# Performance work log

Hardware: AMD Instinct MI355X
Metric: run time of the kernel (lower is better)

Reference implementation:

```python
import jax, jax.numpy as jnp
import numpy as np

B, C, H, W = 2, 256, 48, 48
KD = 256          # key_dim
CLS = 20          # num_classes
NT = H * W        # patch tokens in query
N = CLS + NT      # key length (cls tokens + patches)
HDS = 8           # num_heads
HD = C // HDS     # head_dim
SCALE = HD ** -0.5
MR = 0.3          # mask_ratio
EPS = 1e-5


def setup_inputs() -> dict:
    key = jax.random.key(0)
    ks = jax.random.split(key, 10)
    s = 0.02
    return {
        "x_query": jax.random.normal(ks[0], (B, C, H, W), jnp.float32),
        "x_key": jax.random.normal(ks[1], (B, N, KD), jnp.float32),
        "mask_u": jax.random.uniform(ks[2], (B, HDS, N, N), jnp.float32),
        "g1": jnp.ones((C,), jnp.float32), "be1": jnp.zeros((C,), jnp.float32),
        "g2": jnp.ones((KD,), jnp.float32), "be2": jnp.zeros((KD,), jnp.float32),
        "g3": jnp.ones((C,), jnp.float32), "be3": jnp.zeros((C,), jnp.float32),
        "Wq": jax.random.normal(ks[3], (C, C), jnp.float32) * s,
        "Wkv": jax.random.normal(ks[4], (KD, 2 * C), jnp.float32) * s,
        "Wcls": jax.random.normal(ks[5], (KD, C), jnp.float32) * s,
        "Wp": jax.random.normal(ks[6], (C, C), jnp.float32) * s,
        "bp": jnp.zeros((C,), jnp.float32),
        "W1": jax.random.normal(ks[7], (C, 4 * C), jnp.float32) * s,
        "bf1": jnp.zeros((4 * C,), jnp.float32),
        "W2": jax.random.normal(ks[8], (4 * C, C), jnp.float32) * s,
        "bf2": jnp.zeros((C,), jnp.float32),
    }


def _ln(x, g, b):
    m = jnp.mean(x, -1, keepdims=True)
    v = jnp.mean((x - m) ** 2, -1, keepdims=True)
    return (x - m) * jax.lax.rsqrt(v + EPS) * g + b


def reference(x_query, x_key, mask_u, g1, be1, g2, be2, g3, be3,
              Wq, Wkv, Wcls, Wp, bp, W1, bf1, W2, bf2):
    Bb, Cc, Hh, Ww = x_query.shape
    xq = x_query.transpose(0, 2, 3, 1).reshape(Bb, -1, Cc)  # [B, Nt, C]
    q_in = _ln(xq, g1, be1)
    k_in = _ln(x_key, g2, be2)
    # cross attention with cls-token prepend
    cls_t = k_in[:, :CLS] @ Wcls                      # [B, Cls, C]
    qcat = jnp.concatenate([cls_t, q_in @ Wq], 1)     # [B, Cls+Nt, C]
    M = qcat.shape[1]
    Nk = x_key.shape[1]
    q = qcat.reshape(Bb, M, HDS, HD).transpose(0, 2, 1, 3)        # [B,h,M,d]
    kv = (k_in @ Wkv).reshape(Bb, Nk, 2, HDS, HD).transpose(2, 0, 3, 1, 4)
    k, v = kv[0], kv[1]                                           # [B,h,N,d]
    attn = jnp.einsum('bhmd,bhnd->bhmn', q, k) * SCALE            # [B,h,M,N]
    # split softmax: cls columns and patch columns normalized separately
    attn = jnp.concatenate([
        jax.nn.softmax(attn[..., :CLS], axis=-1),
        jax.nn.softmax(attn[..., CLS:], axis=-1),
    ], axis=-1)
    # stochastic bernoulli(mask_ratio) mask -> -1e12, then re-softmax
    bern = (mask_u < MR).astype(attn.dtype)
    attn = jax.nn.softmax(attn + bern * (-1e12), axis=-1)
    x = jnp.einsum('bhmn,bhnd->bhmd', attn, v)
    x = x.transpose(0, 2, 1, 3).reshape(Bb, M, Cc)
    x = x @ Wp + bp
    x = x[:, CLS:]                                    # drop cls rows
    xq = xq + x                                       # residual 1
    h = jax.nn.gelu(_ln(xq, g3, be3) @ W1 + bf1, approximate=False)
    xq = xq + (h @ W2 + bf2)                          # residual 2 (MLP)
    return xq.transpose(0, 2, 1).reshape(Bb, Cc, Hh, Ww)
```

## Files before the change

kernel.cpp:

```cpp
#include <hip/hip_runtime.h>
#include <hip/hip_bf16.h>
#include <cstddef>

#define B_ 2
#define C_ 256
#define HW_ 2304
#define CLS_ 20
#define N_ 2324
#define HDS_ 8
#define HD_ 32
#define SCALE_F 0.17677669529663687f
#define MR_ 0.3f
#define EPS_ 1e-5f
#define NT64 37
#define NPAD 2368

typedef __attribute__((ext_vector_type(8))) short short8;
typedef __attribute__((ext_vector_type(4))) float f32x4;
typedef unsigned long long u64;

__device__ __forceinline__ short f2bf(float x) {
    union { __hip_bfloat16 b; short s; } u;
    u.b = __float2bfloat16(x);
    return u.s;
}
__device__ __forceinline__ u64 shfl_xor_u64(u64 v, int m) {
    unsigned lo = (unsigned)v, hi = (unsigned)(v >> 32);
    lo = (unsigned)__shfl_xor((int)lo, m, 64);
    hi = (unsigned)__shfl_xor((int)hi, m, 64);
    return ((u64)hi << 32) | lo;
}

__global__ __launch_bounds__(256) void wtrans_kernel(
    const float* __restrict__ W, short* __restrict__ Wt, int K, int Nn, float scale)
{
    __shared__ float S[32][33];
    int n0 = blockIdx.x * 32, k0 = blockIdx.y * 32;
    int t = threadIdx.x;
    int nl = t & 31, kq = t >> 5;
    #pragma unroll
    for (int ii = 0; ii < 4; ++ii) {
        int k = kq + ii * 8;
        S[k][nl] = W[(size_t)(k0 + k) * Nn + n0 + nl] * scale;
    }
    __syncthreads();
    int kl = t & 31, nq = t >> 5;
    #pragma unroll
    for (int ii = 0; ii < 4; ++ii) {
        int n = nq + ii * 8;
        Wt[(size_t)(n0 + n) * K + k0 + kl] = f2bf(S[kl][n]);
    }
}

__global__ __launch_bounds__(256) void mask_compress_kernel(
    const float* __restrict__ mask, u64* __restrict__ mbits)
{
    int rid = blockIdx.x * 4 + (threadIdx.x >> 6);
    int l = threadIdx.x & 63;
    const float* mrow = mask + (size_t)rid * N_;
    u64* orow = mbits + (size_t)rid * NT64;
    #pragma unroll
    for (int base = 0; base < 10; ++base) {
        int col = base * 256 + l * 4;
        unsigned nib = 0;
        if (col < N_) {
            float4 u = *(const float4*)&mrow[col];
            nib = (u.x >= MR_ ? 1u : 0u) | (u.y >= MR_ ? 2u : 0u)
                | (u.z >= MR_ ? 4u : 0u) | (u.w >= MR_ ? 8u : 0u);
        }
        u64 part = (u64)nib << (4 * (l & 15));
        part |= shfl_xor_u64(part, 1);
        part |= shfl_xor_u64(part, 2);
        part |= shfl_xor_u64(part, 4);
        part |= shfl_xor_u64(part, 8);
        int widx = base * 4 + (l >> 4);
        if ((l & 15) == 0 && widx < NT64) orow[widx] = part;
    }
}

__global__ __launch_bounds__(256) void lnq_kernel(
    const float* __restrict__ x, const float* __restrict__ g,
    const float* __restrict__ be, short* __restrict__ yln,
    float* __restrict__ yraw)
{
    int row = blockIdx.x;
    int b = row / HW_, n = row % HW_;
    int t = threadIdx.x;
    float v = x[((size_t)(b * C_ + t)) * HW_ + n];
    float s = v, s2 = v * v;
    #pragma unroll
    for (int off = 1; off < 64; off <<= 1) {
        s  += __shfl_xor(s,  off, 64);
        s2 += __shfl_xor(s2, off, 64);
    }
    __shared__ float rs[4], rs2[4];
    int w = t >> 6;
    if ((t & 63) == 0) { rs[w] = s; rs2[w] = s2; }
    __syncthreads();
    s  = rs[0] + rs[1] + rs[2] + rs[3];
    s2 = rs2[0] + rs2[1] + rs2[2] + rs2[3];
    float mean = s * (1.f / 256.f);
    float var  = s2 * (1.f / 256.f) - mean * mean;
    float inv  = rsqrtf(var + EPS_);
    yraw[(size_t)row * C_ + t] = v;
    yln [(size_t)row * C_ + t] = f2bf((v - mean) * inv * g[t] + be[t]);
}

__global__ __launch_bounds__(256) void ln_rows_kernel(
    const float* __restrict__ x, const float* __restrict__ g,
    const float* __restrict__ be, short* __restrict__ y)
{
    int row = blockIdx.x;
    int t = threadIdx.x;
    float v = x[(size_t)row * C_ + t];
    float s = v, s2 = v * v;
    #pragma unroll
    for (int off = 1; off < 64; off <<= 1) {
        s  += __shfl_xor(s,  off, 64);
        s2 += __shfl_xor(s2, off, 64);
    }
    __shared__ float rs[4], rs2[4];
    int w = t >> 6;
    if ((t & 63) == 0) { rs[w] = s; rs2[w] = s2; }
    __syncthreads();
    s  = rs[0] + rs[1] + rs[2] + rs[3];
    s2 = rs2[0] + rs2[1] + rs2[2] + rs2[3];
    float mean = s * (1.f / 256.f);
    float var  = s2 * (1.f / 256.f) - mean * mean;
    float inv  = rsqrtf(var + EPS_);
    y[(size_t)row * C_ + t] = f2bf((v - mean) * inv * g[t] + be[t]);
}

__global__ __launch_bounds__(256) void gemm_bf16_kernel(
    const short* __restrict__ A, const short* __restrict__ Wt,
    void* __restrict__ Cc, int M, int Nn, int K,
    const float* __restrict__ bias, const float* __restrict__ res, int flags)
{
    __shared__ short As[64][40];
    __shared__ short Ws[64][40];
    const int t = threadIdx.x, w = t >> 6, l = t & 63;
    const int quad = l >> 4, c16 = l & 15;
    const int m0 = blockIdx.y * 64, n0 = blockIdx.x * 64;
    const int wm = (w >> 1) * 32, wn = (w & 1) * 32;
    const int sr = t >> 2, sk = (t & 3) * 8;
    const f32x4 cz = {0.f, 0.f, 0.f, 0.f};
    f32x4 acc[2][2] = {{cz, cz}, {cz, cz}};
    for (int k0 = 0; k0 < K; k0 += 32) {
        int ga = m0 + sr; if (ga >= M) ga = M - 1;
        short8 av = *(const short8*)&A[(size_t)ga * K + k0 + sk];
        short8 wv = *(const short8*)&Wt[(size_t)(n0 + sr) * K + k0 + sk];
        __syncthreads();
        *(short8*)&As[sr][sk] = av;
        *(short8*)&Ws[sr][sk] = wv;
        __syncthreads();
        short8 af0 = *(const short8*)&As[wm + c16][quad * 8];
        short8 af1 = *(const short8*)&As[wm + 16 + c16][quad * 8];
        short8 bf0 = *(const short8*)&Ws[wn + c16][quad * 8];
        short8 bf1 = *(const short8*)&Ws[wn + 16 + c16][quad * 8];
        acc[0][0] = __builtin_amdgcn_mfma_f32_16x16x32_bf16(af0, bf0, acc[0][0], 0, 0, 0);
        acc[0][1] = __builtin_amdgcn_mfma_f32_16x16x32_bf16(af0, bf1, acc[0][1], 0, 0, 0);
        acc[1][0] = __builtin_amdgcn_mfma_f32_16x16x32_bf16(af1, bf0, acc[1][0], 0, 0, 0);
        acc[1][1] = __builtin_amdgcn_mfma_f32_16x16x32_bf16(af1, bf1, acc[1][1], 0, 0, 0);
    }
    #pragma unroll
    for (int mb = 0; mb < 2; ++mb) {
        #pragma unroll
        for (int nb = 0; nb < 2; ++nb) {
            #pragma unroll
            for (int r = 0; r < 4; ++r) {
                int m = m0 + wm + mb * 16 + quad * 4 + r;
                if (m >= M) continue;
                int n = n0 + wn + nb * 16 + c16;
                float v = acc[mb][nb][r];
                if (bias) v += bias[n];
                if (flags & 1) v = 0.5f * v * (1.f + erff(v * 0.70710678118654752f));
                if (res) v += res[(size_t)m * Nn + n];
                if (flags & 2) ((short*)Cc)[(size_t)m * Nn + n] = f2bf(v);
                else           ((float*)Cc)[(size_t)m * Nn + n] = v;
            }
        }
    }
}

__global__ __launch_bounds__(256) void vtrans_kernel(
    const short* __restrict__ kvb, short* __restrict__ vtb)
{
    __shared__ short S[64][33];
    int n0 = blockIdx.x * 64;
    int bh = blockIdx.y;
    int b = bh >> 3, h = bh & 7;
    int t = threadIdx.x;
    int d = t & 31, i0 = t >> 5;
    #pragma unroll
    for (int ii = 0; ii < 8; ++ii) {
        int n = n0 + i0 + ii * 8;
        short v = 0;
        if (n < N_) v = kvb[((size_t)(b * N_ + n)) * 512 + 256 + h * 32 + d];
        S[i0 + ii * 8][d] = v;
    }
    __syncthreads();
    int nl = t & 63, d0 = t >> 6;
    #pragma unroll
    for (int jj = 0; jj < 8; ++jj) {
        int dd = d0 + jj * 4;
        vtb[(size_t)bh * 32 * NPAD + (size_t)dd * NPAD + n0 + nl] = S[nl][dd];
    }
}

__global__ __launch_bounds__(256) void attn_mfma_kernel(
    const short* __restrict__ qb,
    const short* __restrict__ kvb,
    const short* __restrict__ vtb,
    const u64*  __restrict__ mbits,
    short* __restrict__ ob)
{
    __shared__ short Ks[64][40];
    __shared__ short Vs[32][72];
    __shared__ short Ps[4][16][72];

    const int t = threadIdx.x;
    const int w = t >> 6, l = t & 63;
    const int quad = l >> 4, c16 = l & 15;
    const int bh = blockIdx.y;
    const int b = bh >> 3, h = bh & 7;
    const int mw = blockIdx.x * 64 + w * 16;
    const f32x4 cz = {0.f, 0.f, 0.f, 0.f};

    const short8 aq = *(const short8*)
        &qb[((size_t)(b * HW_ + mw + c16)) * C_ + h * HD_ + quad * 8];

    const int sn = t >> 2;
    const int sd = (t & 3) * 8;
    const int vd = t >> 3;
    const int vj = (t & 7) * 8;

    float l1[4] = {0.f, 0.f, 0.f, 0.f}, l2[4] = {0.f, 0.f, 0.f, 0.f};
    for (int j0 = 0; j0 < N_; j0 += 64) {
        __syncthreads();
        {
            int gn = j0 + sn;
            short8 kk = {0, 0, 0, 0, 0, 0, 0, 0};
            if (gn < N_)
                kk = *(const short8*)&kvb[((size_t)(b * N_ + gn)) * 512 + h * HD_ + sd];
            *(short8*)&Ks[sn][sd] = kk;
        }
        __syncthreads();
        #pragma unroll
        for (int nb = 0; nb < 4; ++nb) {
            short8 bk = *(const short8*)&Ks[nb * 16 + c16][quad * 8];
            f32x4 c = __builtin_amdgcn_mfma_f32_16x16x32_bf16(aq, bk, cz, 0, 0, 0);
            int j = j0 + nb * 16 + c16;
            #pragma unroll
            for (int r = 0; r < 4; ++r) {
                float e = (j < N_) ? __expf(c[r]) : 0.f;
                if (j < CLS_) l1[r] += e; else l2[r] += e;
            }
        }
    }
    float i1[4], i2[4];
    #pragma unroll
    for (int r = 0; r < 4; ++r) {
        float a = l1[r], s = l2[r];
        #pragma unroll
        for (int off = 1; off < 16; off <<= 1) {
            a += __shfl_xor(a, off, 64);
            s += __shfl_xor(s, off, 64);
        }
        i1[r] = 1.f / a;
        i2[r] = 1.f / s;
    }

    f32x4 o0 = cz, o1 = cz;
    float zz[4] = {0.f, 0.f, 0.f, 0.f};
    const u64* mbase = mbits + ((size_t)bh * N_ + (CLS_ + mw + quad * 4)) * NT64;
    for (int j0 = 0; j0 < N_; j0 += 64) {
        __syncthreads();
        {
            int gn = j0 + sn;
            short8 kk = {0, 0, 0, 0, 0, 0, 0, 0};
            if (gn < N_)
                kk = *(const short8*)&kvb[((size_t)(b * N_ + gn)) * 512 + h * HD_ + sd];
            *(short8*)&Ks[sn][sd] = kk;
            *(short8*)&Vs[vd][vj] =
                *(const short8*)&vtb[(size_t)bh * 32 * NPAD + (size_t)vd * NPAD + j0 + vj];
        }
        u64 wb[4];
        {
            const u64* mp = mbase + (j0 >> 6);
            #pragma unroll
            for (int r = 0; r < 4; ++r) wb[r] = mp[(size_t)r * NT64];
        }
        __syncthreads();
        #pragma unroll
        for (int nb = 0; nb < 4; ++nb) {
            short8 bk = *(const short8*)&Ks[nb * 16 + c16][quad * 8];
            f32x4 c = __builtin_amdgcn_mfma_f32_16x16x32_bf16(aq, bk, cz, 0, 0, 0);
            int j = j0 + nb * 16 + c16;
            float inv = (j < CLS_) ? 0.f : 1.f;
            #pragma unroll
            for (int r = 0; r < 4; ++r) {
                float iv = (j < CLS_) ? i1[r] : i2[r];
                float p = __expf(c[r]) * iv;
                bool keep = (wb[r] >> (nb * 16 + c16)) & 1;
                float wgt = keep ? __expf(p) : 0.f;
                zz[r] += wgt;
                Ps[w][quad * 4 + r][nb * 16 + c16] = f2bf(wgt);
            }
            (void)inv;
        }
        __syncthreads();
        #pragma unroll
        for (int kc = 0; kc < 2; ++kc) {
            short8 ap  = *(const short8*)&Ps[w][c16][kc * 32 + quad * 8];
            short8 bv0 = *(const short8*)&Vs[c16][kc * 32 + quad * 8];
            short8 bv1 = *(const short8*)&Vs[16 + c16][kc * 32 + quad * 8];
            o0 = __builtin_amdgcn_mfma_f32_16x16x32_bf16(ap, bv0, o0, 0, 0, 0);
            o1 = __builtin_amdgcn_mfma_f32_16x16x32_bf16(ap, bv1, o1, 0, 0, 0);
        }
    }
    #pragma unroll
    for (int r = 0; r < 4; ++r) {
        float z = zz[r];
        #pragma unroll
        for (int off = 1; off < 16; off <<= 1) z += __shfl_xor(z, off, 64);
        float iz = 1.f / z;
        size_t orow = (size_t)(b * HW_ + mw + quad * 4 + r) * C_ + h * HD_;
        ob[orow + c16]      = f2bf(o0[r] * iz);
        ob[orow + 16 + c16] = f2bf(o1[r] * iz);
    }
}

__global__ __launch_bounds__(256) void transpose_kernel(
    const float* __restrict__ y, float* __restrict__ out)
{
    __shared__ float tile[64][65];
    int n0 = blockIdx.x * 64, c0 = blockIdx.y * 64, b = blockIdx.z;
    int lc = threadIdx.x & 63, lr = threadIdx.x >> 6;
    #pragma unroll
    for (int i = lr; i < 64; i += 4)
        tile[lc][i] = y[((size_t)(b * HW_ + n0 + i)) * C_ + c0 + lc];
    __syncthreads();
    #pragma unroll
    for (int i = lr; i < 64; i += 4)
        out[((size_t)(b * C_ + c0 + i)) * HW_ + n0 + lc] = tile[i][lc];
}

extern "C" void kernel_launch(void* const* d_in, const int* in_sizes, int n_in,
                              void* d_out, int out_size, void* d_ws, size_t ws_size,
                              hipStream_t stream)
{
    const float* x_query = (const float*)d_in[0];
    const float* x_key   = (const float*)d_in[1];
    const float* mask_u  = (const float*)d_in[2];
    const float* g1  = (const float*)d_in[3];
    const float* be1 = (const float*)d_in[4];
    const float* g2  = (const float*)d_in[5];
    const float* be2 = (const float*)d_in[6];
    const float* g3  = (const float*)d_in[7];
    const float* be3 = (const float*)d_in[8];
    const float* Wq  = (const float*)d_in[9];
    const float* Wkv = (const float*)d_in[10];
    const float* Wp  = (const float*)d_in[12];
    const float* bp  = (const float*)d_in[13];
    const float* W1  = (const float*)d_in[14];
    const float* bf1 = (const float*)d_in[15];
    const float* W2  = (const float*)d_in[16];
    const float* bf2 = (const float*)d_in[17];
    float* out = (float*)d_out;

    char* p = (char*)d_ws;
    short* Wq_t  = (short*)p; p += (size_t)256 * 256 * 2;
    short* Wkv_t = (short*)p; p += (size_t)512 * 256 * 2;
    short* Wp_t  = (short*)p; p += (size_t)256 * 256 * 2;
    short* W1_t  = (short*)p; p += (size_t)1024 * 256 * 2;
    short* W2_t  = (short*)p; p += (size_t)256 * 1024 * 2;
    u64*  mbits  = (u64*)p;   p += (size_t)16 * N_ * NT64 * 8;
    float* xq_t  = (float*)p; p += (size_t)B_ * HW_ * C_ * 4;
    short* q_in  = (short*)p; p += (size_t)B_ * HW_ * C_ * 2;
    short* k_in  = (short*)p; p += (size_t)B_ * N_ * C_ * 2;
    short* q_buf = (short*)p; p += (size_t)B_ * HW_ * C_ * 2;
    short* kv_b  = (short*)p; p += (size_t)B_ * N_ * 512 * 2;
    short* vt_b  = (short*)p; p += (size_t)16 * 32 * NPAD * 2;
    float* xq2   = (float*)p; p += (size_t)B_ * HW_ * C_ * 4;
    short* o_buf = q_in;
    short* ln3   = k_in;
    short* h_buf = (short*)mbits;
    float* y_buf = (float*)q_buf;

    wtrans_kernel<<<dim3(256 / 32, 256 / 32), 256, 0, stream>>>(Wq, Wq_t, 256, 256, SCALE_F);
    wtrans_kernel<<<dim3(512 / 32, 256 / 32), 256, 0, stream>>>(Wkv, Wkv_t, 256, 512, 1.f);
    wtrans_kernel<<<dim3(256 / 32, 256 / 32), 256, 0, stream>>>(Wp, Wp_t, 256, 256, 1.f);
    wtrans_kernel<<<dim3(1024 / 32, 256 / 32), 256, 0, stream>>>(W1, W1_t, 256, 1024, 1.f);
    wtrans_kernel<<<dim3(256 / 32, 1024 / 32), 256, 0, stream>>>(W2, W2_t, 1024, 256, 1.f);
    mask_compress_kernel<<<(16 * N_) / 4, 256, 0, stream>>>(mask_u, mbits);
    lnq_kernel<<<B_ * HW_, 256, 0, stream>>>(x_query, g1, be1, q_in, xq_t);
    ln_rows_kernel<<<B_ * N_, 256, 0, stream>>>(x_key, g2, be2, k_in);
    gemm_bf16_kernel<<<dim3(C_ / 64, (B_ * HW_) / 64), 256, 0, stream>>>(
        q_in, Wq_t, q_buf, B_ * HW_, C_, C_, nullptr, nullptr, 2);
    gemm_bf16_kernel<<<dim3(512 / 64, (B_ * N_ + 63) / 64), 256, 0, stream>>>(
        k_in, Wkv_t, kv_b, B_ * N_, 512, C_, nullptr, nullptr, 2);
    vtrans_kernel<<<dim3(NT64, 16), 256, 0, stream>>>(kv_b, vt_b);
    attn_mfma_kernel<<<dim3(HW_ / 64, B_ * HDS_), 256, 0, stream>>>(
        q_buf, kv_b, vt_b, mbits, o_buf);
    gemm_bf16_kernel<<<dim3(C_ / 64, (B_ * HW_) / 64), 256, 0, stream>>>(
        o_buf, Wp_t, xq2, B_ * HW_, C_, C_, bp, xq_t, 0);
    ln_rows_kernel<<<B_ * HW_, 256, 0, stream>>>(xq2, g3, be3, ln3);
    gemm_bf16_kernel<<<dim3(1024 / 64, (B_ * HW_) / 64), 256, 0, stream>>>(
        ln3, W1_t, h_buf, B_ * HW_, 1024, C_, bf1, nullptr, 3);
    gemm_bf16_kernel<<<dim3(C_ / 64, (B_ * HW_) / 64), 256, 0, stream>>>(
        h_buf, W2_t, y_buf, B_ * HW_, C_, 1024, bf2, xq2, 0);
    transpose_kernel<<<dim3(HW_ / 64, C_ / 64, B_), 256, 0, stream>>>(y_buf, out);
}
```

Before: 720.5 us.

## Prefetch next tiles into registers in GEMM and attention, merge weight transposes

Adds register double-buffering of the next K/V and A/W tiles in the attention and GEMM loops, so global loads overlap with MFMA work on the current tile. Merges the five weight-transpose launches into one kernel, batches the mask loads ahead of the bit packing, and drops a block barrier before the per-wave P·V step. This raises register pressure, and the dropped barrier depends on Ps being private to each wave.

```diff
diff --git a/kernel.cpp b/kernel.cpp
--- a/kernel.cpp
+++ b/kernel.cpp
@@ -31,11 +31,24 @@
     return ((u64)hi << 32) | lo;
 }
 
-__global__ __launch_bounds__(256) void wtrans_kernel(
-    const float* __restrict__ W, short* __restrict__ Wt, int K, int Nn, float scale)
+__global__ __launch_bounds__(256) void wtrans_all_kernel(
+    const float* __restrict__ Wq,  const float* __restrict__ Wkv,
+    const float* __restrict__ Wp,  const float* __restrict__ W1,
+    const float* __restrict__ W2,
+    short* __restrict__ Wq_t, short* __restrict__ Wkv_t,
+    short* __restrict__ Wp_t, short* __restrict__ W1_t,
+    short* __restrict__ W2_t)
 {
     __shared__ float S[32][33];
-    int n0 = blockIdx.x * 32, k0 = blockIdx.y * 32;
+    int bid = blockIdx.x;
+    const float* W; short* Wt; int K, Nn; float scale;
+    if (bid < 64)       { W = Wq;  Wt = Wq_t;  K = 256;  Nn = 256;  scale = SCALE_F; }
+    else if (bid < 192) { bid -= 64;  W = Wkv; Wt = Wkv_t; K = 256;  Nn = 512;  scale = 1.f; }
+    else if (bid < 256) { bid -= 192; W = Wp;  Wt = Wp_t;  K = 256;  Nn = 256;  scale = 1.f; }
+    else if (bid < 512) { bid -= 256; W = W1;  Wt = W1_t;  K = 256;  Nn = 1024; scale = 1.f; }
+    else                { bid -= 512; W = W2;  Wt = W2_t;  K = 1024; Nn = 256;  scale = 1.f; }
+    int nblk = Nn / 32;
+    int n0 = (bid % nblk) * 32, k0 = (bid / nblk) * 32;
     int t = threadIdx.x;
     int nl = t & 31, kq = t >> 5;
     #pragma unroll
@@ -59,15 +72,18 @@
     int l = threadIdx.x & 63;
     const float* mrow = mask + (size_t)rid * N_;
     u64* orow = mbits + (size_t)rid * NT64;
+    float4 uu[10];
     #pragma unroll
     for (int base = 0; base < 10; ++base) {
         int col = base * 256 + l * 4;
-        unsigned nib = 0;
-        if (col < N_) {
-            float4 u = *(const float4*)&mrow[col];
-            nib = (u.x >= MR_ ? 1u : 0u) | (u.y >= MR_ ? 2u : 0u)
-                | (u.z >= MR_ ? 4u : 0u) | (u.w >= MR_ ? 8u : 0u);
-        }
+        if (col < N_) uu[base] = *(const float4*)&mrow[col];
+        else { uu[base].x = -1.f; uu[base].y = -1.f; uu[base].z = -1.f; uu[base].w = -1.f; }
+    }
+    #pragma unroll
+    for (int base = 0; base < 10; ++base) {
+        float4 u = uu[base];
+        unsigned nib = (u.x >= MR_ ? 1u : 0u) | (u.y >= MR_ ? 2u : 0u)
+                     | (u.z >= MR_ ? 4u : 0u) | (u.w >= MR_ ? 8u : 0u);
         u64 part = (u64)nib << (4 * (l & 15));
         part |= shfl_xor_u64(part, 1);
         part |= shfl_xor_u64(part, 2);
@@ -145,13 +161,17 @@
     const int sr = t >> 2, sk = (t & 3) * 8;
     const f32x4 cz = {0.f, 0.f, 0.f, 0.f};
     f32x4 acc[2][2] = {{cz, cz}, {cz, cz}};
+    int ga = m0 + sr; if (ga >= M) ga = M - 1;
+    short8 av = *(const short8*)&A[(size_t)ga * K + sk];
+    short8 wv = *(const short8*)&Wt[(size_t)(n0 + sr) * K + sk];
     for (int k0 = 0; k0 < K; k0 += 32) {
-        int ga = m0 + sr; if (ga >= M) ga = M - 1;
-        short8 av = *(const short8*)&A[(size_t)ga * K + k0 + sk];
-        short8 wv = *(const short8*)&Wt[(size_t)(n0 + sr) * K + k0 + sk];
         __syncthreads();
         *(short8*)&As[sr][sk] = av;
         *(short8*)&Ws[sr][sk] = wv;
+        if (k0 + 32 < K) {
+            av = *(const short8*)&A[(size_t)ga * K + k0 + 32 + sk];
+            wv = *(const short8*)&Wt[(size_t)(n0 + sr) * K + k0 + 32 + sk];
+        }
         __syncthreads();
         short8 af0 = *(const short8*)&As[wm + c16][quad * 8];
         short8 af1 = *(const short8*)&As[wm + 16 + c16][quad * 8];
@@ -235,14 +255,18 @@
     const int vj = (t & 7) * 8;
 
     float l1[4] = {0.f, 0.f, 0.f, 0.f}, l2[4] = {0.f, 0.f, 0.f, 0.f};
+    short8 kk = {0, 0, 0, 0, 0, 0, 0, 0};
+    if (sn < N_)
+        kk = *(const short8*)&kvb[((size_t)(b * N_ + sn)) * 512 + h * HD_ + sd];
     for (int j0 = 0; j0 < N_; j0 += 64) {
         __syncthreads();
-        {
-            int gn = j0 + sn;
-            short8 kk = {0, 0, 0, 0, 0, 0, 0, 0};
+        *(short8*)&Ks[sn][sd] = kk;
+        if (j0 + 64 < N_) {
+            int gn = j0 + 64 + sn;
+            short8 nk = {0, 0, 0, 0, 0, 0, 0, 0};
             if (gn < N_)
-                kk = *(const short8*)&kvb[((size_t)(b * N_ + gn)) * 512 + h * HD_ + sd];
-            *(short8*)&Ks[sn][sd] = kk;
+                nk = *(const short8*)&kvb[((size_t)(b * N_ + gn)) * 512 + h * HD_ + sd];
+            kk = nk;
         }
         __syncthreads();
         #pragma unroll
@@ -273,16 +297,22 @@
     f32x4 o0 = cz, o1 = cz;
     float zz[4] = {0.f, 0.f, 0.f, 0.f};
     const u64* mbase = mbits + ((size_t)bh * N_ + (CLS_ + mw + quad * 4)) * NT64;
+    const size_t vrow = (size_t)bh * 32 * NPAD + (size_t)vd * NPAD + vj;
+    short8 kk2 = {0, 0, 0, 0, 0, 0, 0, 0};
+    if (sn < N_)
+        kk2 = *(const short8*)&kvb[((size_t)(b * N_ + sn)) * 512 + h * HD_ + sd];
+    short8 vv = *(const short8*)&vtb[vrow];
     for (int j0 = 0; j0 < N_; j0 += 64) {
         __syncthreads();
-        {
-            int gn = j0 + sn;
-            short8 kk = {0, 0, 0, 0, 0, 0, 0, 0};
+        *(short8*)&Ks[sn][sd] = kk2;
+        *(short8*)&Vs[vd][vj] = vv;
+        if (j0 + 64 < N_) {
+            int gn = j0 + 64 + sn;
+            short8 nk = {0, 0, 0, 0, 0, 0, 0, 0};
             if (gn < N_)
-                kk = *(const short8*)&kvb[((size_t)(b * N_ + gn)) * 512 + h * HD_ + sd];
-            *(short8*)&Ks[sn][sd] = kk;
-            *(short8*)&Vs[vd][vj] =
-                *(const short8*)&vtb[(size_t)bh * 32 * NPAD + (size_t)vd * NPAD + j0 + vj];
+                nk = *(const short8*)&kvb[((size_t)(b * N_ + gn)) * 512 + h * HD_ + sd];
+            kk2 = nk;
+            vv = *(const short8*)&vtb[vrow + j0 + 64];
         }
         u64 wb[4];
         {
@@ -296,7 +326,6 @@
             short8 bk = *(const short8*)&Ks[nb * 16 + c16][quad * 8];
             f32x4 c = __builtin_amdgcn_mfma_f32_16x16x32_bf16(aq, bk, cz, 0, 0, 0);
             int j = j0 + nb * 16 + c16;
-            float inv = (j < CLS_) ? 0.f : 1.f;
             #pragma unroll
             for (int r = 0; r < 4; ++r) {
                 float iv = (j < CLS_) ? i1[r] : i2[r];
@@ -306,9 +335,7 @@
                 zz[r] += wgt;
                 Ps[w][quad * 4 + r][nb * 16 + c16] = f2bf(wgt);
             }
-            (void)inv;
-        }
-        __syncthreads();
+        }
         #pragma unroll
         for (int kc = 0; kc < 2; ++kc) {
             short8 ap  = *(const short8*)&Ps[w][c16][kc * 32 + quad * 8];
@@ -387,11 +414,8 @@
     short* h_buf = (short*)mbits;
     float* y_buf = (float*)q_buf;
 
-    wtrans_kernel<<<dim3(256 / 32, 256 / 32), 256, 0, stream>>>(Wq, Wq_t, 256, 256, SCALE_F);
-    wtrans_kernel<<<dim3(512 / 32, 256 / 32), 256, 0, stream>>>(Wkv, Wkv_t, 256, 512, 1.f);
-    wtrans_kernel<<<dim3(256 / 32, 256 / 32), 256, 0, stream>>>(Wp, Wp_t, 256, 256, 1.f);
-    wtrans_kernel<<<dim3(1024 / 32, 256 / 32), 256, 0, stream>>>(W1, W1_t, 256, 1024, 1.f);
-    wtrans_kernel<<<dim3(256 / 32, 1024 / 32), 256, 0, stream>>>(W2, W2_t, 1024, 256, 1.f);
+    wtrans_all_kernel<<<768, 256, 0, stream>>>(
+        Wq, Wkv, Wp, W1, W2, Wq_t, Wkv_t, Wp_t, W1_t, W2_t);
     mask_compress_kernel<<<(16 * N_) / 4, 256, 0, stream>>>(mask_u, mbits);
     lnq_kernel<<<B_ * HW_, 256, 0, stream>>>(x_query, g1, be1, q_in, xq_t);
     ln_rows_kernel<<<B_ * N_, 256, 0, stream>>>(x_key, g2, be2, k_in);
```

After: 689.1 us. -4.3%, faster.
